# Optimization experiments

Hardware: AMD Instinct MI355X
Metric: run time of the kernel (lower is better)

The kernel has to match this reference:

```python
import jax, jax.numpy as jnp
import numpy as np

D_MODEL = 2048
NUM_HEADS = 16
D_K = D_MODEL // NUM_HEADS
B, S, PAST = 2, 1024, 3072


def setup_inputs() -> dict:
    key = jax.random.key(0)
    ks = jax.random.split(key, 12)
    s = 1.0 / np.sqrt(D_MODEL)
    inp = {
        "x": jax.random.normal(ks[0], (B, S, D_MODEL), dtype=jnp.float32),
        "past_key": jax.random.normal(ks[1], (B, NUM_HEADS, PAST, D_K), dtype=jnp.float32),
        "past_value": jax.random.normal(ks[2], (B, NUM_HEADS, PAST, D_K), dtype=jnp.float32),
        "Wq": jax.random.normal(ks[3], (D_MODEL, D_MODEL), dtype=jnp.float32) * s,
        "bq": jax.random.normal(ks[4], (D_MODEL,), dtype=jnp.float32) * s,
        "Wk": jax.random.normal(ks[5], (D_MODEL, D_MODEL), dtype=jnp.float32) * s,
        "bk": jax.random.normal(ks[6], (D_MODEL,), dtype=jnp.float32) * s,
        "Wv": jax.random.normal(ks[7], (D_MODEL, D_MODEL), dtype=jnp.float32) * s,
        "bv": jax.random.normal(ks[8], (D_MODEL,), dtype=jnp.float32) * s,
        "Wo": jax.random.normal(ks[9], (D_MODEL, D_MODEL), dtype=jnp.float32) * s,
        "bo": jax.random.normal(ks[10], (D_MODEL,), dtype=jnp.float32) * s,
    }
    return inp


def reference(x, past_key, past_value, Wq, bq, Wk, bk, Wv, bv, Wo, bo):
    b, s, _ = x.shape
    # torch nn.Linear: y = x @ W^T + b
    def proj(W, bias):
        y = jnp.einsum('bsd,ed->bse', x, W) + bias
        return y.reshape(b, s, NUM_HEADS, D_K).transpose(0, 2, 1, 3)  # [B,H,S,dk]
    Q = proj(Wq, bq)
    K = proj(Wk, bk)
    V = proj(Wv, bv)
    K = jnp.concatenate([past_key, K], axis=2)   # [B,H,PAST+S,dk]
    V = jnp.concatenate([past_value, V], axis=2)
    scale = 1.0 / np.sqrt(D_K).astype(np.float32)
    scores = jnp.einsum('bhqd,bhkd->bhqk', Q, K) * scale
    attn = jax.nn.softmax(scores, axis=-1)
    out = jnp.einsum('bhqk,bhkd->bhqd', attn, V)          # [B,H,S,dk]
    out = out.transpose(0, 2, 1, 3).reshape(b, s, D_MODEL)
    out = jnp.einsum('bsd,ed->bse', out, Wo) + bo
    return out, K, V
```

## Files before the change

kernel.cpp:

```cpp
#include <hip/hip_runtime.h>
#include <stdint.h>

typedef __bf16 bf16;
typedef __bf16 bf16x4 __attribute__((ext_vector_type(4)));
typedef __bf16 bf16x8 __attribute__((ext_vector_type(8)));
typedef float  f32x4  __attribute__((ext_vector_type(4)));

#define DMODEL 2048
#define NH 16
#define DK 128
#define SS 1024
#define PASTLEN 3072
#define LTOT 4096
#define KVTILES 64
#define NSPLIT 4
#define NT 16

__device__ __forceinline__ void gload16(const void* g, void* l) {
    __builtin_amdgcn_global_load_lds(
        (__attribute__((address_space(1))) void*)(uintptr_t)g,
        (__attribute__((address_space(3))) void*)(uintptr_t)l,
        16, 0, 0);
}

__global__ __launch_bounds__(256) void cvt5_k(
    const float* __restrict__ s0, const float* __restrict__ s1,
    const float* __restrict__ s2, const float* __restrict__ s3,
    const float* __restrict__ s4,
    bf16* __restrict__ d0, bf16* __restrict__ d1, bf16* __restrict__ d2,
    bf16* __restrict__ d3, bf16* __restrict__ d4, int n8)
{
    const float* s; bf16* d;
    switch (blockIdx.y) {
        case 0: s = s0; d = d0; break;
        case 1: s = s1; d = d1; break;
        case 2: s = s2; d = d2; break;
        case 3: s = s3; d = d3; break;
        default: s = s4; d = d4; break;
    }
    int stride = gridDim.x * blockDim.x;
    for (int i = blockIdx.x*blockDim.x + threadIdx.x; i < n8; i += stride) {
        const float4* p = (const float4*)s + (size_t)i*2;
        float4 a = p[0], b = p[1];
        bf16x8 o;
        o[0]=(bf16)a.x; o[1]=(bf16)a.y; o[2]=(bf16)a.z; o[3]=(bf16)a.w;
        o[4]=(bf16)b.x; o[5]=(bf16)b.y; o[6]=(bf16)b.z; o[7]=(bf16)b.w;
        *((bf16x8*)d + i) = o;
    }
}

__global__ __launch_bounds__(256) void gemm_bt(
    const bf16* __restrict__ A,
    const bf16* __restrict__ W0, const bf16* __restrict__ W1, const bf16* __restrict__ W2,
    const float* __restrict__ b0, const float* __restrict__ b1, const float* __restrict__ b2,
    bf16* __restrict__ outQ, float* __restrict__ outK, float* __restrict__ outV,
    float* __restrict__ outO, int mode)
{
    __shared__ __align__(16) bf16 As[128*32];
    __shared__ __align__(16) bf16 Bs[128*32];
    const int tid  = threadIdx.x;
    const int wave = tid >> 6, lane = tid & 63;
    const int l15 = lane & 15, l4 = lane >> 4;
    int which, ntile;
    if (mode == 0) { which = blockIdx.y >> 4; ntile = blockIdx.y & 15; }
    else           { which = 3;               ntile = blockIdx.y; }
    const bf16*  W    = (mode != 0 || which == 0) ? W0 : (which == 1 ? W1 : W2);
    const float* bias = (mode != 0 || which == 0) ? b0 : (which == 1 ? b1 : b2);
    const int m0 = blockIdx.x * 128, n0 = ntile * 128;
    const int wm = wave >> 1, wn = wave & 1;

    f32x4 acc[4][4] = {};

    for (int k0 = 0; k0 < DMODEL; k0 += 32) {
        __syncthreads();
        #pragma unroll
        for (int c = 0; c < 2; ++c) {
            const int base = c*4096 + wave*1024;
            const int byte = base + lane*16;
            const int row  = byte >> 6;
            const int ke   = (byte & 63) >> 1;
            gload16(A + (size_t)(m0+row)*DMODEL + k0 + ke, (char*)As + base);
            gload16(W + (size_t)(n0+row)*DMODEL + k0 + ke, (char*)Bs + base);
        }
        asm volatile("s_waitcnt vmcnt(0)" ::: "memory");
        __syncthreads();
        bf16x8 af[4], bfv[4];
        #pragma unroll
        for (int mf = 0; mf < 4; ++mf)
            af[mf] = *(const bf16x8*)((const char*)As + (wm*64 + mf*16 + l15)*64 + l4*16);
        #pragma unroll
        for (int nf = 0; nf < 4; ++nf)
            bfv[nf] = *(const bf16x8*)((const char*)Bs + (wn*64 + nf*16 + l15)*64 + l4*16);
        #pragma unroll
        for (int mf = 0; mf < 4; ++mf)
            #pragma unroll
            for (int nf = 0; nf < 4; ++nf)
                acc[mf][nf] = __builtin_amdgcn_mfma_f32_16x16x32_bf16(af[mf], bfv[nf], acc[mf][nf], 0, 0, 0);
    }

    float bv4[4];
    #pragma unroll
    for (int nf = 0; nf < 4; ++nf) bv4[nf] = bias[n0 + wn*64 + nf*16 + l15];

    const int rbase = m0 + wm*64 + l4*4;
    const int cbase = n0 + wn*64 + l15;

    if (mode == 1) {
        #pragma unroll
        for (int mf = 0; mf < 4; ++mf)
        #pragma unroll
        for (int nf = 0; nf < 4; ++nf) {
            const int col = cbase + nf*16;
            #pragma unroll
            for (int r = 0; r < 4; ++r) {
                const int row = rbase + mf*16 + r;
                outO[(size_t)row*DMODEL + col] = acc[mf][nf][r] + bv4[nf];
            }
        }
    } else if (which == 0) {
        const float qs = 0.08838834764831845f * 1.4426950408889634f;
        #pragma unroll
        for (int mf = 0; mf < 4; ++mf)
        #pragma unroll
        for (int nf = 0; nf < 4; ++nf) {
            const int col = cbase + nf*16;
            const int h = col >> 7, d = col & 127;
            #pragma unroll
            for (int r = 0; r < 4; ++r) {
                const int row = rbase + mf*16 + r;
                const int b = row >> 10, s = row & 1023;
                outQ[((size_t)(b*NH + h)*SS + s)*DK + d] = (bf16)((acc[mf][nf][r] + bv4[nf]) * qs);
            }
        }
    } else {
        float* dst = (which == 1) ? outK : outV;
        #pragma unroll
        for (int mf = 0; mf < 4; ++mf)
        #pragma unroll
        for (int nf = 0; nf < 4; ++nf) {
            const int col = cbase + nf*16;
            const int h = col >> 7, d = col & 127;
            #pragma unroll
            for (int r = 0; r < 4; ++r) {
                const int row = rbase + mf*16 + r;
                const int b = row >> 10, s = row & 1023;
                dst[((size_t)(b*NH + h)*LTOT + PASTLEN + s)*DK + d] = acc[mf][nf][r] + bv4[nf];
            }
        }
    }
}

__global__ __launch_bounds__(256) void kvprep_k(
    const float* __restrict__ pk, const float* __restrict__ pv,
    float* __restrict__ Kf, float* __restrict__ Vf,
    bf16* __restrict__ Kb, bf16* __restrict__ Vb)
{
    __shared__ float Vt_f[64*132];
    const int tid = threadIdx.x;
    const int tau = blockIdx.x, bh = blockIdx.y;
    const bool past = tau < 48;
    const size_t srcoff = past ? ((size_t)bh*PASTLEN + tau*64)*DK
                               : ((size_t)bh*LTOT    + tau*64)*DK;
    const float* srcK = (past ? pk : Kf) + srcoff;
    const float* srcV = (past ? pv : Vf) + srcoff;
    float* dstKf = Kf + ((size_t)bh*LTOT + tau*64)*DK;
    float* dstVf = Vf + ((size_t)bh*LTOT + tau*64)*DK;
    char* kblob = (char*)Kb + (((size_t)bh*KVTILES + tau) << 14);
    char* vblob = (char*)Vb + (((size_t)bh*KVTILES + tau) << 14);

    #pragma unroll
    for (int i = 0; i < 8; ++i) {
        const int f4 = i*256 + tid;
        const int r  = f4 >> 5;
        const int c8 = f4 & 31;
        float4 k4 = ((const float4*)srcK)[f4];
        float4 v4 = ((const float4*)srcV)[f4];
        if (past) {
            ((float4*)dstKf)[f4] = k4;
            ((float4*)dstVf)[f4] = v4;
        }
        bf16x4 kq; kq[0]=(bf16)k4.x; kq[1]=(bf16)k4.y; kq[2]=(bf16)k4.z; kq[3]=(bf16)k4.w;
        *(bf16x4*)(kblob + r*256 + ((c8*8) ^ ((r&7)<<4))) = kq;
        *(float4*)&Vt_f[r*132 + c8*4] = v4;
    }
    __syncthreads();
    const int d = tid >> 1, half = tid & 1;
    const int dx = (d & 7) << 4;
    #pragma unroll
    for (int jj = 0; jj < 4; ++jj) {
        const int chunk = half*4 + jj;
        bf16x8 o;
        #pragma unroll
        for (int e = 0; e < 8; ++e) {
            const int j  = chunk*8 + e;
            const int oe = ((j & 31) >> 1) + ((j & 1) << 4) + (j & 32);
            o[e] = (bf16)Vt_f[oe*132 + d];
        }
        *(bf16x8*)(vblob + d*128 + ((chunk*16) ^ dx)) = o;
    }
}

__global__ __launch_bounds__(512, 2) void attn_k(
    const bf16* __restrict__ Qb,
    const bf16* __restrict__ Kb, const bf16* __restrict__ Vb,
    bf16* __restrict__ Opart, float* __restrict__ Marr, float* __restrict__ Larr)
{
    __shared__ __align__(16) char KL[2][16384];
    __shared__ __align__(16) char VL[2][16384];
    __shared__ __align__(16) char PsL[8][2048];

    const int tid  = threadIdx.x;
    const int wave = tid >> 6, lane = tid & 63;
    const int l15 = lane & 15, l4 = lane >> 4;
    const int wgid = blockIdx.x;
    const int qt = (wgid >> 3) & 3;
    const int g  = ((wgid >> 5) << 3) | (wgid & 7);
    const int bh = g >> 2, sp = g & 3;
    const int qbase = qt*256 + wave*32;

    bf16x8 qf[2][4];
    #pragma unroll
    for (int qq = 0; qq < 2; ++qq) {
        const bf16* qptr = Qb + ((size_t)bh*SS + qbase + qq*16 + l15)*DK;
        #pragma unroll
        for (int ks = 0; ks < 4; ++ks)
            qf[qq][ks] = *(const bf16x8*)(qptr + ks*32 + l4*8);
    }

    const char* kblobs = (const char*)Kb + (((size_t)bh*KVTILES + sp*NT) << 14);
    const char* vblobs = (const char*)Vb + (((size_t)bh*KVTILES + sp*NT) << 14);
    char* myPs = PsL[wave];
    const int soff = wave*2048;

    bf16x8 ones8;
    #pragma unroll
    for (int e = 0; e < 8; ++e) ones8[e] = (bf16)1.0f;

    float m_run[2][4];
    f32x4 oacc[2][8];
    f32x4 lacc[2];
    #pragma unroll
    for (int qq = 0; qq < 2; ++qq) {
        #pragma unroll
        for (int r = 0; r < 4; ++r) m_run[qq][r] = -1e30f;
        #pragma unroll
        for (int df = 0; df < 8; ++df) oacc[qq][df] = f32x4{0.f,0.f,0.f,0.f};
        lacc[qq] = f32x4{0.f,0.f,0.f,0.f};
    }

    #pragma unroll
    for (int c = 0; c < 2; ++c) {
        gload16(kblobs + soff + c*1024 + lane*16, KL[0] + soff + c*1024);
        gload16(vblobs + soff + c*1024 + lane*16, VL[0] + soff + c*1024);
    }

    for (int t = 0; t < NT; ++t) {
        const int cur = t & 1;
        if (t + 1 < NT) {
            const char* kb = kblobs + ((size_t)(t+1) << 14);
            const char* vb = vblobs + ((size_t)(t+1) << 14);
            #pragma unroll
            for (int c = 0; c < 2; ++c) {
                gload16(kb + soff + c*1024 + lane*16, KL[cur^1] + soff + c*1024);
                gload16(vb + soff + c*1024 + lane*16, VL[cur^1] + soff + c*1024);
            }
            asm volatile("s_waitcnt vmcnt(4)" ::: "memory");
        } else {
            asm volatile("s_waitcnt vmcnt(0)" ::: "memory");
        }
        __builtin_amdgcn_s_barrier();

        const char* Kc = KL[cur];
        const char* Vc = VL[cur];

        f32x4 sa[2][4];
        #pragma unroll
        for (int qq = 0; qq < 2; ++qq)
            #pragma unroll
            for (int nf = 0; nf < 4; ++nf) sa[qq][nf] = f32x4{0.f,0.f,0.f,0.f};
        __builtin_amdgcn_s_setprio(1);
        #pragma unroll
        for (int nf = 0; nf < 4; ++nf) {
            const int krow = nf*16 + l15;
            const int rx = (krow & 7) << 4;
            #pragma unroll
            for (int ks = 0; ks < 4; ++ks) {
                bf16x8 kf = *(const bf16x8*)(Kc + krow*256 + ((ks*64 + l4*16) ^ rx));
                sa[0][nf] = __builtin_amdgcn_mfma_f32_16x16x32_bf16(qf[0][ks], kf, sa[0][nf], 0,0,0);
                sa[1][nf] = __builtin_amdgcn_mfma_f32_16x16x32_bf16(qf[1][ks], kf, sa[1][nf], 0,0,0);
            }
        }
        __builtin_amdgcn_s_setprio(0);

        float mt[2][4];
        bool ok = true;
        #pragma unroll
        for (int qq = 0; qq < 2; ++qq)
            #pragma unroll
            for (int r = 0; r < 4; ++r) {
                float m0 = fmaxf(fmaxf(sa[qq][0][r], sa[qq][1][r]),
                                 fmaxf(sa[qq][2][r], sa[qq][3][r]));
                #pragma unroll
                for (int off = 1; off < 16; off <<= 1) m0 = fmaxf(m0, __shfl_xor(m0, off, 64));
                mt[qq][r] = m0;
                ok = ok && (m0 <= m_run[qq][r] + 8.0f);
            }
        if (!__all(ok)) {
            #pragma unroll
            for (int qq = 0; qq < 2; ++qq)
                #pragma unroll
                for (int r = 0; r < 4; ++r) {
                    const float mn   = fmaxf(m_run[qq][r], mt[qq][r]);
                    const float corr = exp2f(m_run[qq][r] - mn);
                    m_run[qq][r] = mn;
                    #pragma unroll
                    for (int df = 0; df < 8; ++df) oacc[qq][df][r] *= corr;
                    lacc[qq][r] *= corr;
                }
        }

        bf16x8 pf[2][2];
        #pragma unroll
        for (int h = 0; h < 2; ++h) {
            #pragma unroll
            for (int qq = 0; qq < 2; ++qq)
                #pragma unroll
                for (int r = 0; r < 4; ++r) {
                    union { bf16 b[2]; uint32_t u; } pk2;
                    pk2.b[0] = (bf16)exp2f(sa[qq][2*h  ][r] - m_run[qq][r]);
                    pk2.b[1] = (bf16)exp2f(sa[qq][2*h+1][r] - m_run[qq][r]);
                    const int row = qq*16 + l4*4 + r;
                    *(uint32_t*)(myPs + row*64 + ((l15*4) ^ ((row&3)<<4))) = pk2.u;
                }
            #pragma unroll
            for (int qq = 0; qq < 2; ++qq) {
                const int prow = qq*16 + l15;
                pf[qq][h] = *(const bf16x8*)(myPs + prow*64 + ((l4*16) ^ ((prow&3)<<4)));
            }
        }

        __builtin_amdgcn_s_setprio(1);
        #pragma unroll
        for (int ks2 = 0; ks2 < 2; ++ks2) {
            lacc[0] = __builtin_amdgcn_mfma_f32_16x16x32_bf16(pf[0][ks2], ones8, lacc[0], 0,0,0);
            lacc[1] = __builtin_amdgcn_mfma_f32_16x16x32_bf16(pf[1][ks2], ones8, lacc[1], 0,0,0);
            #pragma unroll
            for (int df = 0; df < 8; ++df) {
                const int d = df*16 + l15;
                bf16x8 vf = *(const bf16x8*)(Vc + d*128 + ((ks2*64 + l4*16) ^ ((d&7)<<4)));
                oacc[0][df] = __builtin_amdgcn_mfma_f32_16x16x32_bf16(pf[0][ks2], vf, oacc[0][df], 0,0,0);
                oacc[1][df] = __builtin_amdgcn_mfma_f32_16x16x32_bf16(pf[1][ks2], vf, oacc[1][df], 0,0,0);
            }
        }
        __builtin_amdgcn_s_setprio(0);

        __builtin_amdgcn_s_barrier();
    }

    bf16* op = Opart + ((size_t)sp*32 + bh)*SS*DK;
    #pragma unroll
    for (int qq = 0; qq < 2; ++qq)
        #pragma unroll
        for (int df = 0; df < 8; ++df)
            #pragma unroll
            for (int r = 0; r < 4; ++r) {
                const int q = qbase + qq*16 + l4*4 + r;
                op[(size_t)q*DK + df*16 + l15] = (bf16)oacc[qq][df][r];
            }
    if (l15 == 0) {
        #pragma unroll
        for (int qq = 0; qq < 2; ++qq)
            #pragma unroll
            for (int r = 0; r < 4; ++r) {
                const int q = qbase + qq*16 + l4*4 + r;
                Marr[(size_t)sp*32768 + bh*SS + q] = m_run[qq][r];
                Larr[(size_t)sp*32768 + bh*SS + q] = lacc[qq][r];
            }
    }
}

__global__ __launch_bounds__(256) void combine_k(
    const bf16* __restrict__ Opart, const float* __restrict__ Marr,
    const float* __restrict__ Larr, bf16* __restrict__ Ob)
{
    const int gid = blockIdx.x*256 + threadIdx.x;
    const int row = gid >> 4;
    const int c8  = gid & 15;
    const int bh = row >> 10, q = row & 1023;
    float m[NSPLIT], l[NSPLIT];
    #pragma unroll
    for (int s = 0; s < NSPLIT; ++s) {
        m[s] = Marr[(size_t)s*32768 + row];
        l[s] = Larr[(size_t)s*32768 + row];
    }
    float M = m[0];
    #pragma unroll
    for (int s = 1; s < NSPLIT; ++s) M = fmaxf(M, m[s]);
    float w[NSPLIT], den = 0.f;
    #pragma unroll
    for (int s = 0; s < NSPLIT; ++s) { w[s] = exp2f(m[s] - M); den += l[s]*w[s]; }
    const float inv = 1.f / den;
    #pragma unroll
    for (int s = 0; s < NSPLIT; ++s) w[s] *= inv;
    float acc[8] = {};
    #pragma unroll
    for (int s = 0; s < NSPLIT; ++s) {
        bf16x8 p = *(const bf16x8*)(Opart + (size_t)s*4194304 + (size_t)row*DK + c8*8);
        #pragma unroll
        for (int e = 0; e < 8; ++e) acc[e] += (float)p[e]*w[s];
    }
    const int b = bh >> 4, h = bh & 15;
    bf16x8 o;
    #pragma unroll
    for (int e = 0; e < 8; ++e) o[e] = (bf16)acc[e];
    *(bf16x8*)(Ob + ((size_t)(b*SS + q))*DMODEL + h*DK + c8*8) = o;
}

extern "C" void kernel_launch(void* const* d_in, const int* in_sizes, int n_in,
                              void* d_out, int out_size, void* d_ws, size_t ws_size,
                              hipStream_t stream) {
    const float* x  = (const float*)d_in[0];
    const float* pk = (const float*)d_in[1];
    const float* pv = (const float*)d_in[2];
    const float* Wq = (const float*)d_in[3];
    const float* bq = (const float*)d_in[4];
    const float* Wk = (const float*)d_in[5];
    const float* bk = (const float*)d_in[6];
    const float* Wv = (const float*)d_in[7];
    const float* bv = (const float*)d_in[8];
    const float* Wo = (const float*)d_in[9];
    const float* bo = (const float*)d_in[10];

    float* out  = (float*)d_out;
    float* Kout = out + 4194304;
    float* Vout = out + 20971520;

    char* ws = (char*)d_ws;
    bf16* xb    = (bf16*)(ws);
    bf16* Wqb   = (bf16*)(ws + (size_t)8*1024*1024);
    bf16* Wkb   = (bf16*)(ws + (size_t)16*1024*1024);
    bf16* Wvb   = (bf16*)(ws + (size_t)24*1024*1024);
    bf16* Wob   = (bf16*)(ws + (size_t)32*1024*1024);
    bf16* Qb    = (bf16*)(ws + (size_t)40*1024*1024);
    bf16* Ob    = (bf16*)(ws + (size_t)48*1024*1024);
    bf16* Kb    = (bf16*)(ws + (size_t)56*1024*1024);
    bf16* Vb    = (bf16*)(ws + (size_t)88*1024*1024);
    bf16*  Opart = (bf16*)(ws);
    float* Marr  = out;
    float* Larr  = out + 131072;

    cvt5_k<<<dim3(1024, 5), 256, 0, stream>>>(x, Wq, Wk, Wv, Wo,
                                              xb, Wqb, Wkb, Wvb, Wob, 524288);
    gemm_bt<<<dim3(16, 48), 256, 0, stream>>>(xb, Wqb, Wkb, Wvb, bq, bk, bv,
                                              Qb, Kout, Vout, nullptr, 0);
    kvprep_k<<<dim3(64, 32), 256, 0, stream>>>(pk, pv, Kout, Vout, Kb, Vb);
    attn_k<<<512, 512, 0, stream>>>(Qb, Kb, Vb, Opart, Marr, Larr);
    combine_k<<<2048, 256, 0, stream>>>(Opart, Marr, Larr, Ob);
    gemm_bt<<<dim3(16, 16), 256, 0, stream>>>(Ob, Wob, nullptr, nullptr, bo, nullptr, nullptr,
                                              nullptr, nullptr, nullptr, out, 1);
}
```

Before: 316.0 us.

## Compute transposed QK^T so P stays in registers, drop LDS P round-trip

Swaps the MFMA operand order for the score computation so each lane holds a query column, letting the exponentiated scores be packed directly into the A-operand layout for the PV MFMA without writing P through shared memory. The V blob permutation is changed to match the new key ordering inside P fragments. Row max reduction now uses two cross-lane shuffles instead of four, and per-row correction factors are broadcast via shuffle when rescaling. This removes the per-tile LDS store/load of P and its shared buffer, in exchange for extra shuffles on the rescale path and a tighter coupling between the V layout and the register layout.

```diff
diff --git a/kernel.cpp b/kernel.cpp
--- a/kernel.cpp
+++ b/kernel.cpp
@@ -193,7 +193,7 @@
         #pragma unroll
         for (int e = 0; e < 8; ++e) {
             const int j  = chunk*8 + e;
-            const int oe = ((j & 31) >> 1) + ((j & 1) << 4) + (j & 32);
+            const int oe = (j & 32) + ((j & 4) << 2) + (((j >> 3) & 3) << 2) + (j & 3);
             o[e] = (bf16)Vt_f[oe*132 + d];
         }
         *(bf16x8*)(vblob + d*128 + ((chunk*16) ^ dx)) = o;
@@ -207,7 +207,6 @@
 {
     __shared__ __align__(16) char KL[2][16384];
     __shared__ __align__(16) char VL[2][16384];
-    __shared__ __align__(16) char PsL[8][2048];
 
     const int tid  = threadIdx.x;
     const int wave = tid >> 6, lane = tid & 63;
@@ -229,20 +228,18 @@
 
     const char* kblobs = (const char*)Kb + (((size_t)bh*KVTILES + sp*NT) << 14);
     const char* vblobs = (const char*)Vb + (((size_t)bh*KVTILES + sp*NT) << 14);
-    char* myPs = PsL[wave];
     const int soff = wave*2048;
 
     bf16x8 ones8;
     #pragma unroll
     for (int e = 0; e < 8; ++e) ones8[e] = (bf16)1.0f;
 
-    float m_run[2][4];
+    float m_run[2];
     f32x4 oacc[2][8];
     f32x4 lacc[2];
+    m_run[0] = -1e30f; m_run[1] = -1e30f;
     #pragma unroll
     for (int qq = 0; qq < 2; ++qq) {
-        #pragma unroll
-        for (int r = 0; r < 4; ++r) m_run[qq][r] = -1e30f;
         #pragma unroll
         for (int df = 0; df < 8; ++df) oacc[qq][df] = f32x4{0.f,0.f,0.f,0.f};
         lacc[qq] = f32x4{0.f,0.f,0.f,0.f};
@@ -286,58 +283,52 @@
             #pragma unroll
             for (int ks = 0; ks < 4; ++ks) {
                 bf16x8 kf = *(const bf16x8*)(Kc + krow*256 + ((ks*64 + l4*16) ^ rx));
-                sa[0][nf] = __builtin_amdgcn_mfma_f32_16x16x32_bf16(qf[0][ks], kf, sa[0][nf], 0,0,0);
-                sa[1][nf] = __builtin_amdgcn_mfma_f32_16x16x32_bf16(qf[1][ks], kf, sa[1][nf], 0,0,0);
+                sa[0][nf] = __builtin_amdgcn_mfma_f32_16x16x32_bf16(kf, qf[0][ks], sa[0][nf], 0,0,0);
+                sa[1][nf] = __builtin_amdgcn_mfma_f32_16x16x32_bf16(kf, qf[1][ks], sa[1][nf], 0,0,0);
             }
         }
         __builtin_amdgcn_s_setprio(0);
 
-        float mt[2][4];
-        bool ok = true;
-        #pragma unroll
-        for (int qq = 0; qq < 2; ++qq)
-            #pragma unroll
-            for (int r = 0; r < 4; ++r) {
-                float m0 = fmaxf(fmaxf(sa[qq][0][r], sa[qq][1][r]),
-                                 fmaxf(sa[qq][2][r], sa[qq][3][r]));
-                #pragma unroll
-                for (int off = 1; off < 16; off <<= 1) m0 = fmaxf(m0, __shfl_xor(m0, off, 64));
-                mt[qq][r] = m0;
-                ok = ok && (m0 <= m_run[qq][r] + 8.0f);
-            }
+        float mt[2];
+        #pragma unroll
+        for (int qq = 0; qq < 2; ++qq) {
+            float a0 = fmaxf(fmaxf(sa[qq][0][0], sa[qq][0][1]), fmaxf(sa[qq][0][2], sa[qq][0][3]));
+            float a1 = fmaxf(fmaxf(sa[qq][1][0], sa[qq][1][1]), fmaxf(sa[qq][1][2], sa[qq][1][3]));
+            float a2 = fmaxf(fmaxf(sa[qq][2][0], sa[qq][2][1]), fmaxf(sa[qq][2][2], sa[qq][2][3]));
+            float a3 = fmaxf(fmaxf(sa[qq][3][0], sa[qq][3][1]), fmaxf(sa[qq][3][2], sa[qq][3][3]));
+            float v = fmaxf(fmaxf(a0, a1), fmaxf(a2, a3));
+            v = fmaxf(v, __shfl_xor(v, 16, 64));
+            v = fmaxf(v, __shfl_xor(v, 32, 64));
+            mt[qq] = v;
+        }
+        const bool ok = (mt[0] <= m_run[0] + 8.0f) && (mt[1] <= m_run[1] + 8.0f);
         if (!__all(ok)) {
             #pragma unroll
-            for (int qq = 0; qq < 2; ++qq)
+            for (int qq = 0; qq < 2; ++qq) {
+                const float mn   = fmaxf(m_run[qq], mt[qq]);
+                const float corr = exp2f(m_run[qq] - mn);
+                m_run[qq] = mn;
                 #pragma unroll
                 for (int r = 0; r < 4; ++r) {
-                    const float mn   = fmaxf(m_run[qq][r], mt[qq][r]);
-                    const float corr = exp2f(m_run[qq][r] - mn);
-                    m_run[qq][r] = mn;
+                    const float c = __shfl(corr, (lane & 48) | (l4*4 + r), 64);
+                    lacc[qq][r] *= c;
                     #pragma unroll
-                    for (int df = 0; df < 8; ++df) oacc[qq][df][r] *= corr;
-                    lacc[qq][r] *= corr;
+                    for (int df = 0; df < 8; ++df) oacc[qq][df][r] *= c;
                 }
+            }
         }
 
         bf16x8 pf[2][2];
         #pragma unroll
-        for (int h = 0; h < 2; ++h) {
-            #pragma unroll
-            for (int qq = 0; qq < 2; ++qq)
+        for (int qq = 0; qq < 2; ++qq)
+            #pragma unroll
+            for (int ks2 = 0; ks2 < 2; ++ks2) {
+                bf16x8 v;
                 #pragma unroll
-                for (int r = 0; r < 4; ++r) {
-                    union { bf16 b[2]; uint32_t u; } pk2;
-                    pk2.b[0] = (bf16)exp2f(sa[qq][2*h  ][r] - m_run[qq][r]);
-                    pk2.b[1] = (bf16)exp2f(sa[qq][2*h+1][r] - m_run[qq][r]);
-                    const int row = qq*16 + l4*4 + r;
-                    *(uint32_t*)(myPs + row*64 + ((l15*4) ^ ((row&3)<<4))) = pk2.u;
-                }
-            #pragma unroll
-            for (int qq = 0; qq < 2; ++qq) {
-                const int prow = qq*16 + l15;
-                pf[qq][h] = *(const bf16x8*)(myPs + prow*64 + ((l4*16) ^ ((prow&3)<<4)));
-            }
-        }
+                for (int e = 0; e < 8; ++e)
+                    v[e] = (bf16)exp2f(sa[qq][ks2*2 + (e >> 2)][e & 3] - m_run[qq]);
+                pf[qq][ks2] = v;
+            }
 
         __builtin_amdgcn_s_setprio(1);
         #pragma unroll
@@ -367,13 +358,17 @@
                 const int q = qbase + qq*16 + l4*4 + r;
                 op[(size_t)q*DK + df*16 + l15] = (bf16)oacc[qq][df][r];
             }
+    if (l4 == 0) {
+        #pragma unroll
+        for (int qq = 0; qq < 2; ++qq)
+            Marr[(size_t)sp*32768 + bh*SS + qbase + qq*16 + l15] = m_run[qq];
+    }
     if (l15 == 0) {
         #pragma unroll
         for (int qq = 0; qq < 2; ++qq)
             #pragma unroll
             for (int r = 0; r < 4; ++r) {
                 const int q = qbase + qq*16 + l4*4 + r;
-                Marr[(size_t)sp*32768 + bh*SS + q] = m_run[qq][r];
                 Larr[(size_t)sp*32768 + bh*SS + q] = lacc[qq][r];
             }
     }
```

Result: faster. 290.8 us (-8.0%).
